# Performance work log

Hardware: AMD Instinct MI355X
Metric: run time of the kernel (lower is better)

## Reference

```python
import jax, jax.numpy as jnp
import numpy as np

B, T, C = 4, 2048, 384
NUM_HEADS, HEAD_SIZE = 6, 64


def setup_inputs() -> dict:
    key = jax.random.key(0)
    ks = jax.random.split(key, 6)
    s = 1.0 / np.sqrt(C)
    return {
        "x": jax.random.normal(ks[0], (B, T, C), dtype=jnp.float32),
        "Wq": jax.random.normal(ks[1], (C, NUM_HEADS * HEAD_SIZE), dtype=jnp.float32) * s,
        "bq": jnp.zeros((NUM_HEADS * HEAD_SIZE,), dtype=jnp.float32),
        "Wk": jax.random.normal(ks[2], (C, NUM_HEADS * HEAD_SIZE), dtype=jnp.float32) * s,
        "bk": jnp.zeros((NUM_HEADS * HEAD_SIZE,), dtype=jnp.float32),
        "Wv": jax.random.normal(ks[3], (C, NUM_HEADS * HEAD_SIZE), dtype=jnp.float32) * s,
        "bv": jnp.zeros((NUM_HEADS * HEAD_SIZE,), dtype=jnp.float32),
        "Wo": jax.random.normal(ks[4], (NUM_HEADS * HEAD_SIZE, C), dtype=jnp.float32) * s,
        "bo": jnp.zeros((C,), dtype=jnp.float32),
    }


def reference(x, Wq, bq, Wk, bk, Wv, bv, Wo, bo):
    b, t, c = x.shape
    h, d = NUM_HEADS, HEAD_SIZE
    q = (x @ Wq + bq).reshape(b, t, h, d)
    k = (x @ Wk + bk).reshape(b, t, h, d)
    v = (x @ Wv + bv).reshape(b, t, h, d)
    scores = jnp.einsum('bthd,bshd->bhts', q, k) / jnp.sqrt(jnp.float32(d))
    causal = jnp.tril(jnp.ones((t, t), dtype=bool))  # [t,t]
    scores = jnp.where(causal, scores, -jnp.inf)
    weights = jax.nn.softmax(scores, axis=-1)  # dropout identity (inference)
    ctx = jnp.einsum('bhts,bshd->bthd', weights, v).reshape(b, t, h * d)
    return ctx @ Wo + bo
```

## Files before the change

kernel.cpp:

```cpp
#include <hip/hip_runtime.h>

#define B_  4
#define T_  2048
#define C_  384
#define NH_ 6
#define HS_ 64
#define M_  (B_*T_)

typedef float floatx4 __attribute__((ext_vector_type(4)));
typedef __bf16 bf16x8 __attribute__((ext_vector_type(8)));
typedef unsigned short ushort_t;
typedef unsigned short ushortx8 __attribute__((ext_vector_type(8)));
typedef unsigned short ushortx4 __attribute__((ext_vector_type(4)));

__device__ __forceinline__ ushort_t f2bf(float f) {
    unsigned u = __builtin_bit_cast(unsigned, f);
    unsigned r = (u + 0x7FFFu + ((u >> 16) & 1u)) >> 16;
    return (ushort_t)r;
}
__device__ __forceinline__ ushort_t f2bf_t(float f) {
    return (ushort_t)(__builtin_bit_cast(unsigned, f) >> 16);
}

__global__ __launch_bounds__(256) void prep(
    const float* __restrict__ x, ushort_t* __restrict__ xb,
    const float* __restrict__ Wq, const float* __restrict__ Wk,
    const float* __restrict__ Wv, const float* __restrict__ Wo,
    ushort_t* __restrict__ Wtq, ushort_t* __restrict__ Wtk,
    ushort_t* __restrict__ Wtv, ushort_t* __restrict__ Wto)
{
    __shared__ float Ls[64][65];
    const int tid = threadIdx.x;
    const int bx = blockIdx.x;

    if (bx < 1536) {
        const int i = (bx * 256 + tid) * 8;
        const float4 a = *(const float4*)&x[i];
        const float4 b = *(const float4*)&x[i + 4];
        ushortx8 p;
        p[0] = f2bf(a.x); p[1] = f2bf(a.y); p[2] = f2bf(a.z); p[3] = f2bf(a.w);
        p[4] = f2bf(b.x); p[5] = f2bf(b.y); p[6] = f2bf(b.z); p[7] = f2bf(b.w);
        *(ushortx8*)&xb[i] = p;
        return;
    }

    const int idx = bx - 1536;
    const int z = idx / 36, rest = idx % 36;
    const float* __restrict__ W = (z == 0) ? Wq : (z == 1) ? Wk : (z == 2) ? Wv : Wo;
    ushort_t* __restrict__ Wt   = (z == 0) ? Wtq : (z == 1) ? Wtk : (z == 2) ? Wtv : Wto;
    const int k0 = (rest / 6) * 64, n0 = (rest % 6) * 64;

    #pragma unroll
    for (int p = 0; p < 4; ++p) {
        const int kk = p * 16 + (tid >> 4);
        const int nn = (tid & 15) * 4;
        const float4 v = *(const float4*)&W[(size_t)(k0 + kk) * 384 + n0 + nn];
        Ls[kk][nn] = v.x; Ls[kk][nn + 1] = v.y; Ls[kk][nn + 2] = v.z; Ls[kk][nn + 3] = v.w;
    }
    __syncthreads();
    #pragma unroll
    for (int p = 0; p < 4; ++p) {
        const int n = p * 16 + (tid >> 4);
        const int kc = (tid & 15) * 4;
        ushortx4 pk;
        #pragma unroll
        for (int t = 0; t < 4; ++t) pk[t] = f2bf(Ls[kc + t][n]);
        *(ushortx4*)&Wt[(size_t)(n0 + n) * 384 + k0 + kc] = pk;
    }
}

__global__ __launch_bounds__(256) void qkv_gemm(
    const ushort_t* __restrict__ xb,
    const ushort_t* __restrict__ Wtq, const ushort_t* __restrict__ Wtk,
    const ushort_t* __restrict__ Wtv,
    const float* __restrict__ bq, const float* __restrict__ bk, const float* __restrict__ bv,
    ushort_t* __restrict__ Qb, ushort_t* __restrict__ Kb, ushort_t* __restrict__ Vtb)
{
    __shared__ ushort_t Sm[2][6144];

    const int tid  = threadIdx.x;
    const int lane = tid & 63;
    const int wv   = tid >> 6;
    const int m    = lane & 15;
    const int quad = lane >> 4;

    const int t0 = blockIdx.x * 64;
    const int n0 = blockIdx.y * 128;
    const int which = n0 / 384;
    const int n_in0 = n0 % 384;
    const bool isV = (which == 2);

    const ushort_t* __restrict__ Wt = (which == 0) ? Wtq : (which == 1) ? Wtk : Wtv;

    const int tg0 = (wv & 1) * 32;
    const int ng0 = (wv >> 1) * 64;

    const int rX = tid >> 2, cX = tid & 3;
    const int swX = ((cX ^ ((rX >> 1) & 3)) << 3);
    const int rW0 = tid >> 2, rW1 = rW0 + 64, cW = tid & 3;
    const int swW = ((cW ^ ((rW0 >> 1) & 3)) << 3);

    floatx4 acc[8];
    #pragma unroll
    for (int i = 0; i < 8; ++i) acc[i] = (floatx4){0.f, 0.f, 0.f, 0.f};

    ushortx8 xr  = *(const ushortx8*)&xb[(size_t)(t0 + rX) * 384 + cX * 8];
    ushortx8 wr0 = *(const ushortx8*)&Wt[(size_t)(n_in0 + rW0) * 384 + cW * 8];
    ushortx8 wr1 = *(const ushortx8*)&Wt[(size_t)(n_in0 + rW1) * 384 + cW * 8];

    for (int ks = 0; ks < 12; ++ks) {
        ushort_t* __restrict__ S = &Sm[ks & 1][0];
        *(ushortx8*)&S[rX * 32 + swX] = xr;
        *(ushortx8*)&S[2048 + rW0 * 32 + swW] = wr0;
        *(ushortx8*)&S[2048 + rW1 * 32 + swW] = wr1;
        __syncthreads();

        if (ks < 11) {
            const int kk = (ks + 1) * 32;
            xr  = *(const ushortx8*)&xb[(size_t)(t0 + rX) * 384 + kk + cX * 8];
            wr0 = *(const ushortx8*)&Wt[(size_t)(n_in0 + rW0) * 384 + kk + cW * 8];
            wr1 = *(const ushortx8*)&Wt[(size_t)(n_in0 + rW1) * 384 + kk + cW * 8];
        }

        bf16x8 fX[2], fW[4];
        #pragma unroll
        for (int i = 0; i < 2; ++i) {
            const int r = tg0 + i * 16 + m;
            fX[i] = *(const bf16x8*)&S[r * 32 + ((quad ^ ((r >> 1) & 3)) << 3)];
        }
        #pragma unroll
        for (int i = 0; i < 4; ++i) {
            const int r = ng0 + i * 16 + m;
            fW[i] = *(const bf16x8*)&S[2048 + r * 32 + ((quad ^ ((r >> 1) & 3)) << 3)];
        }
        if (isV) {
            #pragma unroll
            for (int i = 0; i < 2; ++i)
                #pragma unroll
                for (int j = 0; j < 4; ++j)
                    acc[i * 4 + j] = __builtin_amdgcn_mfma_f32_16x16x32_bf16(fX[i], fW[j], acc[i * 4 + j], 0, 0, 0);
        } else {
            #pragma unroll
            for (int i = 0; i < 4; ++i)
                #pragma unroll
                for (int j = 0; j < 2; ++j)
                    acc[i * 2 + j] = __builtin_amdgcn_mfma_f32_16x16x32_bf16(fW[i], fX[j], acc[i * 2 + j], 0, 0, 0);
        }
    }

    if (!isV) {
        ushort_t* __restrict__ out = (which == 0) ? Qb : Kb;
        const float* __restrict__ bias = (which == 0) ? bq : bk;
        const float scale = (which == 0) ? 0.125f : 1.0f;
        #pragma unroll
        for (int i = 0; i < 4; ++i) {
            const int n_base = n_in0 + ng0 + i * 16 + quad * 4;
            const int h = n_base >> 6, d0 = n_base & 63;
            #pragma unroll
            for (int j = 0; j < 2; ++j) {
                const int tg = t0 + tg0 + j * 16 + m;
                const int b = tg >> 11, tb = tg & (T_ - 1);
                ushortx4 pk;
                #pragma unroll
                for (int r = 0; r < 4; ++r)
                    pk[r] = f2bf((acc[i * 2 + j][r] + bias[n_base + r]) * scale);
                *(ushortx4*)&out[(((size_t)(b * NH_ + h)) * T_ + tb) * HS_ + d0] = pk;
            }
        }
    } else {
        #pragma unroll
        for (int i = 0; i < 2; ++i) {
            const int tgq = t0 + tg0 + i * 16 + quad * 4;
            const int b = tgq >> 11, tb0 = tgq & (T_ - 1);
            #pragma unroll
            for (int j = 0; j < 4; ++j) {
                const int n_l = n_in0 + ng0 + j * 16 + m;
                const int h = n_l >> 6, d = n_l & 63;
                const float bb = bv[n_l];
                ushortx4 pk;
                #pragma unroll
                for (int r = 0; r < 4; ++r) pk[r] = f2bf(acc[i * 4 + j][r] + bb);
                *(ushortx4*)&Vtb[(((size_t)(b * NH_ + h)) * HS_ + d) * T_ + tb0] = pk;
            }
        }
    }
}

__global__ __launch_bounds__(256) void proj_gemm(
    const ushort_t* __restrict__ ctxb,
    const ushort_t* __restrict__ Wto,
    const float* __restrict__ bo,
    float* __restrict__ out)
{
    __shared__ ushort_t Sm[2][4096];

    const int tid  = threadIdx.x;
    const int lane = tid & 63;
    const int wv   = tid >> 6;
    const int m    = lane & 15;
    const int quad = lane >> 4;

    const int t0 = blockIdx.x * 64;
    const int n0 = blockIdx.y * 64;
    const int tg0 = (wv & 1) * 32;
    const int ng0 = (wv >> 1) * 32;

    const int rC = tid >> 2, cC = tid & 3;
    const int swC = ((cC ^ ((rC >> 1) & 3)) << 3);

    floatx4 acc[2][2];
    #pragma unroll
    for (int i = 0; i < 2; ++i)
        #pragma unroll
        for (int j = 0; j < 2; ++j) acc[i][j] = (floatx4){0.f, 0.f, 0.f, 0.f};

    ushortx8 cr = *(const ushortx8*)&ctxb[(size_t)(t0 + rC) * 384 + cC * 8];
    ushortx8 wr = *(const ushortx8*)&Wto[(size_t)(n0 + rC) * 384 + cC * 8];

    for (int ks = 0; ks < 12; ++ks) {
        ushort_t* __restrict__ S = &Sm[ks & 1][0];
        *(ushortx8*)&S[rC * 32 + swC] = cr;
        *(ushortx8*)&S[2048 + rC * 32 + swC] = wr;
        __syncthreads();

        if (ks < 11) {
            const int kk = (ks + 1) * 32;
            cr = *(const ushortx8*)&ctxb[(size_t)(t0 + rC) * 384 + kk + cC * 8];
            wr = *(const ushortx8*)&Wto[(size_t)(n0 + rC) * 384 + kk + cC * 8];
        }

        bf16x8 fA[2], fB[2];
        #pragma unroll
        for (int i = 0; i < 2; ++i) {
            const int rn = ng0 + i * 16 + m;
            fA[i] = *(const bf16x8*)&S[2048 + rn * 32 + ((quad ^ ((rn >> 1) & 3)) << 3)];
            const int rt = tg0 + i * 16 + m;
            fB[i] = *(const bf16x8*)&S[rt * 32 + ((quad ^ ((rt >> 1) & 3)) << 3)];
        }
        #pragma unroll
        for (int i = 0; i < 2; ++i)
            #pragma unroll
            for (int j = 0; j < 2; ++j)
                acc[i][j] = __builtin_amdgcn_mfma_f32_16x16x32_bf16(fA[i], fB[j], acc[i][j], 0, 0, 0);
    }

    #pragma unroll
    for (int i = 0; i < 2; ++i) {
        const int n_base = n0 + ng0 + i * 16 + quad * 4;
        const float4 bb = *(const float4*)&bo[n_base];
        #pragma unroll
        for (int j = 0; j < 2; ++j) {
            const int tg = t0 + tg0 + j * 16 + m;
            float4 o;
            o.x = acc[i][j][0] + bb.x;
            o.y = acc[i][j][1] + bb.y;
            o.z = acc[i][j][2] + bb.z;
            o.w = acc[i][j][3] + bb.w;
            *(float4*)&out[(size_t)tg * 384 + n_base] = o;
        }
    }
}

__global__ __launch_bounds__(256) void attn_mfma(
    const ushort_t* __restrict__ Q,
    const ushort_t* __restrict__ K,
    const ushort_t* __restrict__ Vt,
    ushort_t* __restrict__ ctx)
{
    __shared__ ushort_t Ks[2][64 * 64];
    __shared__ ushort_t Vs[2][64 * 64];
    __shared__ ushort_t Ps[4][16 * 64];

    const int tid  = threadIdx.x;
    const int lane = tid & 63;
    const int wv   = tid >> 6;
    const int m    = lane & 15;
    const int quad = lane >> 4;
    const int cA   = (quad ^ (m & 7)) << 3;

    const int flat = blockIdx.x + 32 * (blockIdx.y + 6 * blockIdx.z);
    const int rr = flat >> 8, ss = flat & 255;
    const int rank = (rr << 8) + ((rr & 1) ? (255 - ss) : ss);
    const int j   = 31 - (rank / 24);
    const int idx = rank % 24;
    const int bh  = idx;
    const int b   = idx / 6, h = idx % 6;

    const int rowbase = j * 64 + wv * 16;
    const int ext = j;

    const ushort_t* __restrict__ Kg = K  + (size_t)bh * (T_ * HS_);
    const ushort_t* __restrict__ Vg = Vt + (size_t)bh * (HS_ * T_);

    const int r0 = tid >> 3,         c0 = tid & 7;
    const int r1 = (tid + 256) >> 3, c1 = tid & 7;
    const int sw0 = ((c0 ^ (r0 & 7)) << 3);
    const int sw1 = ((c1 ^ (r1 & 7)) << 3);

    bf16x8 qf0, qf1;
    {
        const ushort_t* qp = Q + ((size_t)bh * T_ + rowbase + m) * HS_;
        qf0 = *(const bf16x8*)(qp + quad * 8);
        qf1 = *(const bf16x8*)(qp + 32 + quad * 8);
    }

    floatx4 acc_o[4];
    #pragma unroll
    for (int dt = 0; dt < 4; ++dt) acc_o[dt] = (floatx4){0.f, 0.f, 0.f, 0.f};
    float l_lane[4] = {0.f, 0.f, 0.f, 0.f};

    ushort_t* __restrict__ Pw = &Ps[wv][0];

    ushortx8 kr0 = *(const ushortx8*)&Kg[(size_t)r0 * HS_ + c0 * 8];
    ushortx8 kr1 = *(const ushortx8*)&Kg[(size_t)r1 * HS_ + c1 * 8];
    ushortx8 vr0 = *(const ushortx8*)&Vg[(size_t)r0 * T_ + c0 * 8];
    ushortx8 vr1 = *(const ushortx8*)&Vg[(size_t)r1 * T_ + c1 * 8];

    for (int kt = 0; kt <= ext; ++kt) {
        ushort_t* __restrict__ Kc = &Ks[kt & 1][0];
        ushort_t* __restrict__ Vc = &Vs[kt & 1][0];
        *(ushortx8*)&Kc[r0 * 64 + sw0] = kr0;
        *(ushortx8*)&Kc[r1 * 64 + sw1] = kr1;
        *(ushortx8*)&Vc[r0 * 64 + sw0] = vr0;
        *(ushortx8*)&Vc[r1 * 64 + sw1] = vr1;
        __syncthreads();

        if (kt < ext) {
            const int s1 = (kt + 1) * 64;
            kr0 = *(const ushortx8*)&Kg[(size_t)(s1 + r0) * HS_ + c0 * 8];
            kr1 = *(const ushortx8*)&Kg[(size_t)(s1 + r1) * HS_ + c1 * 8];
            vr0 = *(const ushortx8*)&Vg[(size_t)r0 * T_ + s1 + c0 * 8];
            vr1 = *(const ushortx8*)&Vg[(size_t)r1 * T_ + s1 + c1 * 8];
        }

        floatx4 s[4];
        #pragma unroll
        for (int kc = 0; kc < 4; ++kc) {
            const int kb = (kc * 16 + m) * 64;
            bf16x8 k0 = *(const bf16x8*)&Kc[kb + cA];
            bf16x8 k1 = *(const bf16x8*)&Kc[kb + (cA ^ 32)];
            floatx4 a = (floatx4){0.f, 0.f, 0.f, 0.f};
            a = __builtin_amdgcn_mfma_f32_16x16x32_bf16(qf0, k0, a, 0, 0, 0);
            a = __builtin_amdgcn_mfma_f32_16x16x32_bf16(qf1, k1, a, 0, 0, 0);
            s[kc] = a;
        }

        if (kt == ext) {
            #pragma unroll
            for (int kc = 0; kc < 4; ++kc) {
                const int key = kt * 64 + kc * 16 + m;
                #pragma unroll
                for (int r = 0; r < 4; ++r)
                    if (key > rowbase + quad * 4 + r) s[kc][r] = -1e30f;
            }
        }

        const int mc = m >> 3, mp = m & 7;
        #pragma unroll
        for (int r = 0; r < 4; ++r) {
            const int prow = quad * 4 + r;
            const int psw = prow & 7;
            const float p0 = __expf(s[0][r]);
            const float p1 = __expf(s[1][r]);
            const float p2 = __expf(s[2][r]);
            const float p3 = __expf(s[3][r]);
            l_lane[r] += (p0 + p1) + (p2 + p3);
            const int pb = prow * 64 + mp;
            Pw[pb + (((0 + mc) ^ psw) << 3)] = f2bf_t(p0);
            Pw[pb + (((2 + mc) ^ psw) << 3)] = f2bf_t(p1);
            Pw[pb + (((4 + mc) ^ psw) << 3)] = f2bf_t(p2);
            Pw[pb + (((6 + mc) ^ psw) << 3)] = f2bf_t(p3);
        }
        asm volatile("s_waitcnt lgkmcnt(0)" ::: "memory");
        bf16x8 pf0 = *(const bf16x8*)&Pw[m * 64 + cA];
        bf16x8 pf1 = *(const bf16x8*)&Pw[m * 64 + (cA ^ 32)];

        #pragma unroll
        for (int dt = 0; dt < 4; ++dt) {
            const int vb = (dt * 16 + m) * 64;
            bf16x8 v0 = *(const bf16x8*)&Vc[vb + cA];
            bf16x8 v1 = *(const bf16x8*)&Vc[vb + (cA ^ 32)];
            acc_o[dt] = __builtin_amdgcn_mfma_f32_16x16x32_bf16(pf0, v0, acc_o[dt], 0, 0, 0);
            acc_o[dt] = __builtin_amdgcn_mfma_f32_16x16x32_bf16(pf1, v1, acc_o[dt], 0, 0, 0);
        }
    }

    float l[4];
    #pragma unroll
    for (int r = 0; r < 4; ++r) {
        float ls = l_lane[r];
        ls += __shfl_xor(ls, 1, 64);
        ls += __shfl_xor(ls, 2, 64);
        ls += __shfl_xor(ls, 4, 64);
        ls += __shfl_xor(ls, 8, 64);
        l[r] = ls;
    }
    #pragma unroll
    for (int dt = 0; dt < 4; ++dt) {
        #pragma unroll
        for (int r = 0; r < 4; ++r) {
            const int t = rowbase + quad * 4 + r;
            ctx[((size_t)(b * T_) + t) * C_ + h * HS_ + dt * 16 + m] =
                f2bf(acc_o[dt][r] / l[r]);
        }
    }
}

extern "C" void kernel_launch(void* const* d_in, const int* in_sizes, int n_in,
                              void* d_out, int out_size, void* d_ws, size_t ws_size,
                              hipStream_t stream) {
    const float* x  = (const float*)d_in[0];
    const float* Wq = (const float*)d_in[1];
    const float* bq = (const float*)d_in[2];
    const float* Wk = (const float*)d_in[3];
    const float* bk = (const float*)d_in[4];
    const float* Wv = (const float*)d_in[5];
    const float* bv = (const float*)d_in[6];
    const float* Wo = (const float*)d_in[7];
    const float* bo = (const float*)d_in[8];
    float* out = (float*)d_out;

    const size_t per = (size_t)B_ * NH_ * T_ * HS_;
    const size_t wsz = 384 * 384;
    ushort_t* xb  = (ushort_t*)d_ws;
    ushort_t* Wtq = xb + per;
    ushort_t* Wtk = Wtq + wsz;
    ushort_t* Wtv = Wtk + wsz;
    ushort_t* Wto = Wtv + wsz;
    ushort_t* Qb  = Wto + wsz;
    ushort_t* Kb  = Qb + per;
    ushort_t* Vtb = Kb + per;
    ushort_t* ctxb = Vtb + per;

    prep<<<dim3(1536 + 144), 256, 0, stream>>>(
        x, xb, Wq, Wk, Wv, Wo, Wtq, Wtk, Wtv, Wto);

    qkv_gemm<<<dim3(M_ / 64, 1152 / 128), 256, 0, stream>>>(
        xb, Wtq, Wtk, Wtv, bq, bk, bv, Qb, Kb, Vtb);

    attn_mfma<<<dim3(32, NH_, B_), 256, 0, stream>>>(Qb, Kb, Vtb, ctxb);

    proj_gemm<<<dim3(M_ / 64, 384 / 64), 256, 0, stream>>>(ctxb, Wto, bo, out);
}
```

Baseline: 143.5 us.

## Split KV tiles across wave pairs with 32-row tiles and merge partial outputs

The attention kernel now gives each wave 32 query rows instead of 16. Waves are paired so that each wave in a pair handles alternating KV tiles by parity. K and V fragments read from shared memory are reused across two row tiles, which halves LDS fragment traffic per MFMA. At the end, the partial outputs and row sums from the odd-parity waves are passed through shared memory and added into the even-parity waves before normalising and writing. This costs more registers, a bigger per-wave P buffer, an extra reduction step with two barriers, and load imbalance when the tile count is odd.

```diff
diff --git a/kernel.cpp b/kernel.cpp
--- a/kernel.cpp
+++ b/kernel.cpp
@@ -267,9 +267,7 @@
     const ushort_t* __restrict__ Vt,
     ushort_t* __restrict__ ctx)
 {
-    __shared__ ushort_t Ks[2][64 * 64];
-    __shared__ ushort_t Vs[2][64 * 64];
-    __shared__ ushort_t Ps[4][16 * 64];
+    __shared__ ushort_t smem[24576];
 
     const int tid  = threadIdx.x;
     const int lane = tid & 63;
@@ -278,15 +276,18 @@
     const int quad = lane >> 4;
     const int cA   = (quad ^ (m & 7)) << 3;
 
+    const int rh = wv & 1;
+    const int kp = wv >> 1;
+
     const int flat = blockIdx.x + 32 * (blockIdx.y + 6 * blockIdx.z);
     const int rr = flat >> 8, ss = flat & 255;
     const int rank = (rr << 8) + ((rr & 1) ? (255 - ss) : ss);
     const int j   = 31 - (rank / 24);
     const int idx = rank % 24;
+    const int b   = idx / 6, h = idx % 6;
     const int bh  = idx;
-    const int b   = idx / 6, h = idx % 6;
-
-    const int rowbase = j * 64 + wv * 16;
+
+    const int rowbase = j * 64 + rh * 32;
     const int ext = j;
 
     const ushort_t* __restrict__ Kg = K  + (size_t)bh * (T_ * HS_);
@@ -297,19 +298,22 @@
     const int sw0 = ((c0 ^ (r0 & 7)) << 3);
     const int sw1 = ((c1 ^ (r1 & 7)) << 3);
 
-    bf16x8 qf0, qf1;
-    {
-        const ushort_t* qp = Q + ((size_t)bh * T_ + rowbase + m) * HS_;
-        qf0 = *(const bf16x8*)(qp + quad * 8);
-        qf1 = *(const bf16x8*)(qp + 32 + quad * 8);
-    }
-
-    floatx4 acc_o[4];
-    #pragma unroll
-    for (int dt = 0; dt < 4; ++dt) acc_o[dt] = (floatx4){0.f, 0.f, 0.f, 0.f};
-    float l_lane[4] = {0.f, 0.f, 0.f, 0.f};
-
-    ushort_t* __restrict__ Pw = &Ps[wv][0];
+    bf16x8 qf[2][2];
+    #pragma unroll
+    for (int rt = 0; rt < 2; ++rt) {
+        const ushort_t* qp = Q + ((size_t)bh * T_ + rowbase + rt * 16 + m) * HS_;
+        qf[rt][0] = *(const bf16x8*)(qp + quad * 8);
+        qf[rt][1] = *(const bf16x8*)(qp + 32 + quad * 8);
+    }
+
+    floatx4 acc_o[2][4];
+    #pragma unroll
+    for (int rt = 0; rt < 2; ++rt)
+        #pragma unroll
+        for (int dt = 0; dt < 4; ++dt) acc_o[rt][dt] = (floatx4){0.f, 0.f, 0.f, 0.f};
+    float l_lane[2][4] = {{0.f,0.f,0.f,0.f},{0.f,0.f,0.f,0.f}};
+
+    ushort_t* __restrict__ Pw = &smem[16384 + wv * 2048];
 
     ushortx8 kr0 = *(const ushortx8*)&Kg[(size_t)r0 * HS_ + c0 * 8];
     ushortx8 kr1 = *(const ushortx8*)&Kg[(size_t)r1 * HS_ + c1 * 8];
@@ -317,8 +321,8 @@
     ushortx8 vr1 = *(const ushortx8*)&Vg[(size_t)r1 * T_ + c1 * 8];
 
     for (int kt = 0; kt <= ext; ++kt) {
-        ushort_t* __restrict__ Kc = &Ks[kt & 1][0];
-        ushort_t* __restrict__ Vc = &Vs[kt & 1][0];
+        ushort_t* __restrict__ Kc = &smem[(kt & 1) * 4096];
+        ushort_t* __restrict__ Vc = &smem[8192 + (kt & 1) * 4096];
         *(ushortx8*)&Kc[r0 * 64 + sw0] = kr0;
         *(ushortx8*)&Kc[r1 * 64 + sw1] = kr1;
         *(ushortx8*)&Vc[r0 * 64 + sw0] = vr0;
@@ -333,75 +337,118 @@
             vr1 = *(const ushortx8*)&Vg[(size_t)r1 * T_ + s1 + c1 * 8];
         }
 
-        floatx4 s[4];
+        if ((kt & 1) != kp) continue;
+
+        bf16x8 kf[8];
         #pragma unroll
         for (int kc = 0; kc < 4; ++kc) {
             const int kb = (kc * 16 + m) * 64;
-            bf16x8 k0 = *(const bf16x8*)&Kc[kb + cA];
-            bf16x8 k1 = *(const bf16x8*)&Kc[kb + (cA ^ 32)];
-            floatx4 a = (floatx4){0.f, 0.f, 0.f, 0.f};
-            a = __builtin_amdgcn_mfma_f32_16x16x32_bf16(qf0, k0, a, 0, 0, 0);
-            a = __builtin_amdgcn_mfma_f32_16x16x32_bf16(qf1, k1, a, 0, 0, 0);
-            s[kc] = a;
-        }
-
-        if (kt == ext) {
+            kf[kc * 2]     = *(const bf16x8*)&Kc[kb + cA];
+            kf[kc * 2 + 1] = *(const bf16x8*)&Kc[kb + (cA ^ 32)];
+        }
+
+        const int mc = m >> 3, mp = m & 7;
+        #pragma unroll
+        for (int rt = 0; rt < 2; ++rt) {
+            floatx4 s[4];
             #pragma unroll
             for (int kc = 0; kc < 4; ++kc) {
-                const int key = kt * 64 + kc * 16 + m;
-                #pragma unroll
-                for (int r = 0; r < 4; ++r)
-                    if (key > rowbase + quad * 4 + r) s[kc][r] = -1e30f;
-            }
-        }
-
-        const int mc = m >> 3, mp = m & 7;
-        #pragma unroll
-        for (int r = 0; r < 4; ++r) {
-            const int prow = quad * 4 + r;
-            const int psw = prow & 7;
-            const float p0 = __expf(s[0][r]);
-            const float p1 = __expf(s[1][r]);
-            const float p2 = __expf(s[2][r]);
-            const float p3 = __expf(s[3][r]);
-            l_lane[r] += (p0 + p1) + (p2 + p3);
-            const int pb = prow * 64 + mp;
-            Pw[pb + (((0 + mc) ^ psw) << 3)] = f2bf_t(p0);
-            Pw[pb + (((2 + mc) ^ psw) << 3)] = f2bf_t(p1);
-            Pw[pb + (((4 + mc) ^ psw) << 3)] = f2bf_t(p2);
-            Pw[pb + (((6 + mc) ^ psw) << 3)] = f2bf_t(p3);
+                floatx4 a = (floatx4){0.f, 0.f, 0.f, 0.f};
+                a = __builtin_amdgcn_mfma_f32_16x16x32_bf16(qf[rt][0], kf[kc * 2], a, 0, 0, 0);
+                a = __builtin_amdgcn_mfma_f32_16x16x32_bf16(qf[rt][1], kf[kc * 2 + 1], a, 0, 0, 0);
+                s[kc] = a;
+            }
+            if (kt == ext) {
+                #pragma unroll
+                for (int kc = 0; kc < 4; ++kc) {
+                    const int key = kt * 64 + kc * 16 + m;
+                    #pragma unroll
+                    for (int r = 0; r < 4; ++r)
+                        if (key > rowbase + rt * 16 + quad * 4 + r) s[kc][r] = -1e30f;
+                }
+            }
+            #pragma unroll
+            for (int r = 0; r < 4; ++r) {
+                const int prow = rt * 16 + quad * 4 + r;
+                const int psw = prow & 7;
+                const float p0 = __expf(s[0][r]);
+                const float p1 = __expf(s[1][r]);
+                const float p2 = __expf(s[2][r]);
+                const float p3 = __expf(s[3][r]);
+                l_lane[rt][r] += (p0 + p1) + (p2 + p3);
+                const int pb = prow * 64 + mp;
+                Pw[pb + (((0 + mc) ^ psw) << 3)] = f2bf_t(p0);
+                Pw[pb + (((2 + mc) ^ psw) << 3)] = f2bf_t(p1);
+                Pw[pb + (((4 + mc) ^ psw) << 3)] = f2bf_t(p2);
+                Pw[pb + (((6 + mc) ^ psw) << 3)] = f2bf_t(p3);
+            }
         }
         asm volatile("s_waitcnt lgkmcnt(0)" ::: "memory");
-        bf16x8 pf0 = *(const bf16x8*)&Pw[m * 64 + cA];
-        bf16x8 pf1 = *(const bf16x8*)&Pw[m * 64 + (cA ^ 32)];
-
+
+        bf16x8 vf[8];
         #pragma unroll
         for (int dt = 0; dt < 4; ++dt) {
             const int vb = (dt * 16 + m) * 64;
-            bf16x8 v0 = *(const bf16x8*)&Vc[vb + cA];
-            bf16x8 v1 = *(const bf16x8*)&Vc[vb + (cA ^ 32)];
-            acc_o[dt] = __builtin_amdgcn_mfma_f32_16x16x32_bf16(pf0, v0, acc_o[dt], 0, 0, 0);
-            acc_o[dt] = __builtin_amdgcn_mfma_f32_16x16x32_bf16(pf1, v1, acc_o[dt], 0, 0, 0);
-        }
-    }
-
-    float l[4];
-    #pragma unroll
-    for (int r = 0; r < 4; ++r) {
-        float ls = l_lane[r];
-        ls += __shfl_xor(ls, 1, 64);
-        ls += __shfl_xor(ls, 2, 64);
-        ls += __shfl_xor(ls, 4, 64);
-        ls += __shfl_xor(ls, 8, 64);
-        l[r] = ls;
-    }
-    #pragma unroll
-    for (int dt = 0; dt < 4; ++dt) {
+            vf[dt * 2]     = *(const bf16x8*)&Vc[vb + cA];
+            vf[dt * 2 + 1] = *(const bf16x8*)&Vc[vb + (cA ^ 32)];
+        }
+        #pragma unroll
+        for (int rt = 0; rt < 2; ++rt) {
+            bf16x8 pf0 = *(const bf16x8*)&Pw[(rt * 16 + m) * 64 + cA];
+            bf16x8 pf1 = *(const bf16x8*)&Pw[(rt * 16 + m) * 64 + (cA ^ 32)];
+            #pragma unroll
+            for (int dt = 0; dt < 4; ++dt) {
+                acc_o[rt][dt] = __builtin_amdgcn_mfma_f32_16x16x32_bf16(pf0, vf[dt * 2], acc_o[rt][dt], 0, 0, 0);
+                acc_o[rt][dt] = __builtin_amdgcn_mfma_f32_16x16x32_bf16(pf1, vf[dt * 2 + 1], acc_o[rt][dt], 0, 0, 0);
+            }
+        }
+    }
+
+    float l[2][4];
+    #pragma unroll
+    for (int rt = 0; rt < 2; ++rt)
         #pragma unroll
         for (int r = 0; r < 4; ++r) {
-            const int t = rowbase + quad * 4 + r;
-            ctx[((size_t)(b * T_) + t) * C_ + h * HS_ + dt * 16 + m] =
-                f2bf(acc_o[dt][r] / l[r]);
+            float ls = l_lane[rt][r];
+            ls += __shfl_xor(ls, 1, 64);
+            ls += __shfl_xor(ls, 2, 64);
+            ls += __shfl_xor(ls, 4, 64);
+            ls += __shfl_xor(ls, 8, 64);
+            l[rt][r] = ls;
+        }
+
+    __syncthreads();
+    float* __restrict__ Os = (float*)smem;
+    float* __restrict__ Lp = (float*)smem + 64 * 68;
+    if (kp == 1) {
+        #pragma unroll
+        for (int rt = 0; rt < 2; ++rt) {
+            #pragma unroll
+            for (int dt = 0; dt < 4; ++dt)
+                #pragma unroll
+                for (int r = 0; r < 4; ++r)
+                    Os[(rh * 32 + rt * 16 + quad * 4 + r) * 68 + dt * 16 + m] = acc_o[rt][dt][r];
+            if (m == 0) {
+                #pragma unroll
+                for (int r = 0; r < 4; ++r) Lp[rh * 32 + rt * 16 + quad * 4 + r] = l[rt][r];
+            }
+        }
+    }
+    __syncthreads();
+    if (kp == 0) {
+        #pragma unroll
+        for (int rt = 0; rt < 2; ++rt) {
+            #pragma unroll
+            for (int r = 0; r < 4; ++r) {
+                const int row = rt * 16 + quad * 4 + r;
+                const float lt = l[rt][r] + Lp[rh * 32 + row];
+                const int t = rowbase + row;
+                #pragma unroll
+                for (int dt = 0; dt < 4; ++dt) {
+                    const float o = acc_o[rt][dt][r] + Os[(rh * 32 + row) * 68 + dt * 16 + m];
+                    ctx[((size_t)(b * T_) + t) * C_ + h * HS_ + dt * 16 + m] = f2bf(o / lt);
+                }
+            }
         }
     }
 }
```

Result: slower. 155.7 us (+8.4%).

## Transpose attention MFMA operands so scores and output are key/dim-major per lane

Applied to the files above, without the earlier changes.

Swaps the A/B operands of both MFMAs in the attention kernel so each lane holds one query row's scores across four keys and four output dims. This lets the P tile be written with packed 8-byte LDS stores instead of scattered 2-byte stores. The row-sum reduction drops to two cross-lane shuffles, and the context output is written as 4-element vector stores with a reciprocal multiply instead of per-element divides. The causal mask and swizzled P addressing are rewritten to match the new fragment layout, which carries a risk of indexing mistakes.

```diff
diff --git a/kernel.cpp b/kernel.cpp
--- a/kernel.cpp
+++ b/kernel.cpp
@@ -12,14 +12,16 @@
 typedef unsigned short ushort_t;
 typedef unsigned short ushortx8 __attribute__((ext_vector_type(8)));
 typedef unsigned short ushortx4 __attribute__((ext_vector_type(4)));
+typedef unsigned int uintx2 __attribute__((ext_vector_type(2)));
 
 __device__ __forceinline__ ushort_t f2bf(float f) {
     unsigned u = __builtin_bit_cast(unsigned, f);
     unsigned r = (u + 0x7FFFu + ((u >> 16) & 1u)) >> 16;
     return (ushort_t)r;
 }
-__device__ __forceinline__ ushort_t f2bf_t(float f) {
-    return (ushort_t)(__builtin_bit_cast(unsigned, f) >> 16);
+__device__ __forceinline__ unsigned f2bf_pk(float lo, float hi) {
+    return (__builtin_bit_cast(unsigned, lo) >> 16) |
+           (__builtin_bit_cast(unsigned, hi) & 0xFFFF0000u);
 }
 
 __global__ __launch_bounds__(256) void prep(
@@ -283,11 +285,12 @@
     const int rank = (rr << 8) + ((rr & 1) ? (255 - ss) : ss);
     const int j   = 31 - (rank / 24);
     const int idx = rank % 24;
+    const int b   = idx / 6, h = idx % 6;
     const int bh  = idx;
-    const int b   = idx / 6, h = idx % 6;
 
     const int rowbase = j * 64 + wv * 16;
     const int ext = j;
+    const int qloc = wv * 16 + m;
 
     const ushort_t* __restrict__ Kg = K  + (size_t)bh * (T_ * HS_);
     const ushort_t* __restrict__ Vg = Vt + (size_t)bh * (HS_ * T_);
@@ -307,9 +310,12 @@
     floatx4 acc_o[4];
     #pragma unroll
     for (int dt = 0; dt < 4; ++dt) acc_o[dt] = (floatx4){0.f, 0.f, 0.f, 0.f};
-    float l_lane[4] = {0.f, 0.f, 0.f, 0.f};
+    float l_lane = 0.f;
 
     ushort_t* __restrict__ Pw = &Ps[wv][0];
+    const int pbase = m * 64 + ((quad & 1) << 2);
+    const int pcs   = (quad >> 1);
+    const int pxor  = m & 7;
 
     ushortx8 kr0 = *(const ushortx8*)&Kg[(size_t)r0 * HS_ + c0 * 8];
     ushortx8 kr1 = *(const ushortx8*)&Kg[(size_t)r1 * HS_ + c1 * 8];
@@ -333,44 +339,42 @@
             vr1 = *(const ushortx8*)&Vg[(size_t)r1 * T_ + s1 + c1 * 8];
         }
 
-        floatx4 s[4];
+        floatx4 st[4];
         #pragma unroll
         for (int kc = 0; kc < 4; ++kc) {
             const int kb = (kc * 16 + m) * 64;
             bf16x8 k0 = *(const bf16x8*)&Kc[kb + cA];
             bf16x8 k1 = *(const bf16x8*)&Kc[kb + (cA ^ 32)];
             floatx4 a = (floatx4){0.f, 0.f, 0.f, 0.f};
-            a = __builtin_amdgcn_mfma_f32_16x16x32_bf16(qf0, k0, a, 0, 0, 0);
-            a = __builtin_amdgcn_mfma_f32_16x16x32_bf16(qf1, k1, a, 0, 0, 0);
-            s[kc] = a;
+            a = __builtin_amdgcn_mfma_f32_16x16x32_bf16(k0, qf0, a, 0, 0, 0);
+            a = __builtin_amdgcn_mfma_f32_16x16x32_bf16(k1, qf1, a, 0, 0, 0);
+            st[kc] = a;
         }
 
         if (kt == ext) {
             #pragma unroll
             for (int kc = 0; kc < 4; ++kc) {
-                const int key = kt * 64 + kc * 16 + m;
                 #pragma unroll
                 for (int r = 0; r < 4; ++r)
-                    if (key > rowbase + quad * 4 + r) s[kc][r] = -1e30f;
+                    if (kc * 16 + quad * 4 + r > qloc) st[kc][r] = -1e30f;
             }
         }
 
-        const int mc = m >> 3, mp = m & 7;
-        #pragma unroll
-        for (int r = 0; r < 4; ++r) {
-            const int prow = quad * 4 + r;
-            const int psw = prow & 7;
-            const float p0 = __expf(s[0][r]);
-            const float p1 = __expf(s[1][r]);
-            const float p2 = __expf(s[2][r]);
-            const float p3 = __expf(s[3][r]);
-            l_lane[r] += (p0 + p1) + (p2 + p3);
-            const int pb = prow * 64 + mp;
-            Pw[pb + (((0 + mc) ^ psw) << 3)] = f2bf_t(p0);
-            Pw[pb + (((2 + mc) ^ psw) << 3)] = f2bf_t(p1);
-            Pw[pb + (((4 + mc) ^ psw) << 3)] = f2bf_t(p2);
-            Pw[pb + (((6 + mc) ^ psw) << 3)] = f2bf_t(p3);
-        }
+        float lsum = 0.f;
+        #pragma unroll
+        for (int kc = 0; kc < 4; ++kc) {
+            const float p0 = __expf(st[kc][0]);
+            const float p1 = __expf(st[kc][1]);
+            const float p2 = __expf(st[kc][2]);
+            const float p3 = __expf(st[kc][3]);
+            lsum += (p0 + p1) + (p2 + p3);
+            uintx2 pk;
+            pk[0] = f2bf_pk(p0, p1);
+            pk[1] = f2bf_pk(p2, p3);
+            *(uintx2*)&Pw[pbase + (((kc * 2 + pcs) ^ pxor) << 3)] = pk;
+        }
+        l_lane += lsum;
+
         asm volatile("s_waitcnt lgkmcnt(0)" ::: "memory");
         bf16x8 pf0 = *(const bf16x8*)&Pw[m * 64 + cA];
         bf16x8 pf1 = *(const bf16x8*)&Pw[m * 64 + (cA ^ 32)];
@@ -380,29 +384,24 @@
             const int vb = (dt * 16 + m) * 64;
             bf16x8 v0 = *(const bf16x8*)&Vc[vb + cA];
             bf16x8 v1 = *(const bf16x8*)&Vc[vb + (cA ^ 32)];
-            acc_o[dt] = __builtin_amdgcn_mfma_f32_16x16x32_bf16(pf0, v0, acc_o[dt], 0, 0, 0);
-            acc_o[dt] = __builtin_amdgcn_mfma_f32_16x16x32_bf16(pf1, v1, acc_o[dt], 0, 0, 0);
-        }
-    }
-
-    float l[4];
-    #pragma unroll
-    for (int r = 0; r < 4; ++r) {
-        float ls = l_lane[r];
-        ls += __shfl_xor(ls, 1, 64);
-        ls += __shfl_xor(ls, 2, 64);
-        ls += __shfl_xor(ls, 4, 64);
-        ls += __shfl_xor(ls, 8, 64);
-        l[r] = ls;
-    }
+            acc_o[dt] = __builtin_amdgcn_mfma_f32_16x16x32_bf16(v0, pf0, acc_o[dt], 0, 0, 0);
+            acc_o[dt] = __builtin_amdgcn_mfma_f32_16x16x32_bf16(v1, pf1, acc_o[dt], 0, 0, 0);
+        }
+    }
+
+    float ls = l_lane;
+    ls += __shfl_xor(ls, 16, 64);
+    ls += __shfl_xor(ls, 32, 64);
+    const float rcp = 1.0f / ls;
+
+    const int t = rowbase + m;
+    ushort_t* __restrict__ cp = ctx + ((size_t)(b * T_) + t) * C_ + h * HS_ + quad * 4;
     #pragma unroll
     for (int dt = 0; dt < 4; ++dt) {
-        #pragma unroll
-        for (int r = 0; r < 4; ++r) {
-            const int t = rowbase + quad * 4 + r;
-            ctx[((size_t)(b * T_) + t) * C_ + h * HS_ + dt * 16 + m] =
-                f2bf(acc_o[dt][r] / l[r]);
-        }
+        ushortx4 pk;
+        #pragma unroll
+        for (int r = 0; r < 4; ++r) pk[r] = f2bf(acc_o[dt][r] * rcp);
+        *(ushortx4*)&cp[dt * 16] = pk;
     }
 }
 
```

Measured after the change: 141.6 us. No clear change (-1.3%).
